# Kernel optimization log

Hardware: AMD Instinct MI355X
Metric: run time of the kernel (lower is better)

## Reference

```python
import jax, jax.numpy as jnp
import numpy as np
import math

B, C, H, W = 32, 64, 128, 128  # x has 2*C channels (real||imag)
EPS = 1e-05


def setup_inputs() -> dict:
    key = jax.random.key(0)
    x = jax.random.normal(key, (B, 2 * C, H, W), dtype=jnp.float32)
    g = 1.0 / math.sqrt(2.0)
    gamma = jnp.tile(jnp.array([[g, 0.0], [0.0, g]], dtype=jnp.float32), (C, 1, 1))
    beta = jnp.zeros((C, 2, 1), dtype=jnp.float32)
    return {"x": x, "gamma": gamma, "beta": beta}


def reference(x, gamma, beta):
    # Training-branch complex batchnorm: whiten with inverse sqrt of 2x2 covariance.
    c = gamma.shape[0]
    xr, xi = x[:, :c], x[:, c:]
    mr = jnp.mean(xr, axis=(0, 2, 3), keepdims=True)
    mi = jnp.mean(xi, axis=(0, 2, 3), keepdims=True)
    xrc = xr - mr
    xic = xi - mi
    d = xr.shape[0] * xr.shape[2] * xr.shape[3] - 1  # unbiased denominator
    covRR = jnp.sum(xrc * xrc, axis=(0, 2, 3)) / d
    covII = jnp.sum(xic * xic, axis=(0, 2, 3)) / d
    covRI = jnp.sum(xrc * xic, axis=(0, 2, 3)) / d
    covIR = covRI  # cov(x_imag, x_real) == cov(x_real, x_imag)
    # cov_matrix per torch stacking: M[c] = [[RR, IR], [RI, II]] + eps*I
    m00 = covRR + EPS
    m01 = covIR
    m10 = covRI
    m11 = covII + EPS
    # sqrtm exactly as in source (including its nonstandard t and full-matrix s add)
    tau = m00 + m11
    delta = m00 * m11 - m01 * m10
    s = jnp.sqrt(delta)
    t = jnp.sqrt(tau + 2.0 * delta)
    q00 = (m00 + s) / t
    q01 = (m01 + s) / t
    q10 = (m10 + s) / t
    q11 = (m11 + s) / t
    # closed-form 2x2 inverse of sqrt matrix
    det = q00 * q11 - q01 * q10
    invV = jnp.stack(
        [jnp.stack([q11, -q01], axis=-1), jnp.stack([-q10, q00], axis=-1)],
        axis=-2,
    ) / det[:, None, None]  # (C, 2, 2)
    # fuse gamma @ invV into a single per-channel 2x2 transform
    A = jnp.einsum('cij,cjk->cik', gamma, invV)  # (C, 2, 2)
    a00 = A[:, 0, 0][None, :, None, None]
    a01 = A[:, 0, 1][None, :, None, None]
    a10 = A[:, 1, 0][None, :, None, None]
    a11 = A[:, 1, 1][None, :, None, None]
    b0 = beta[:, 0, 0][None, :, None, None]
    b1 = beta[:, 1, 0][None, :, None, None]
    yr = a00 * xrc + a01 * xic + b0
    yi = a10 * xrc + a11 * xic + b1
    return jnp.concatenate([yr, yi], axis=1)
```

## Files before the change

### kernel.cpp

```cpp
#include <hip/hip_runtime.h>
#include <math.h>

constexpr int B  = 32;
constexpr int C  = 64;
constexpr int H  = 128;
constexpr int W  = 128;
constexpr int HW = H * W;
constexpr int SB = 2 * C * HW;
constexpr float EPS = 1e-5f;

typedef float v4f __attribute__((ext_vector_type(4)));

__global__ __launch_bounds__(256) void k_partial(const float* __restrict__ x,
                                                 float* __restrict__ part) {
    const int c = blockIdx.x;
    const int b = blockIdx.y;
    const float* __restrict__ xr = x + (size_t)b * SB + (size_t)c * HW;
    const float* __restrict__ xi = xr + (size_t)C * HW;
    const int tid = threadIdx.x;

    float sr = 0.f, si = 0.f, srr = 0.f, sii = 0.f, sri = 0.f;

#pragma unroll
    for (int it = 0; it < HW / (256 * 4); ++it) {
        const int idx = (it * 256 + tid) * 4;
        const v4f r = *reinterpret_cast<const v4f*>(xr + idx);
        const v4f i = *reinterpret_cast<const v4f*>(xi + idx);
        sr  += r.x + r.y + r.z + r.w;
        si  += i.x + i.y + i.z + i.w;
        srr += r.x * r.x + r.y * r.y + r.z * r.z + r.w * r.w;
        sii += i.x * i.x + i.y * i.y + i.z * i.z + i.w * i.w;
        sri += r.x * i.x + r.y * i.y + r.z * i.z + r.w * i.w;
    }

#pragma unroll
    for (int off = 32; off > 0; off >>= 1) {
        sr  += __shfl_down(sr,  off);
        si  += __shfl_down(si,  off);
        srr += __shfl_down(srr, off);
        sii += __shfl_down(sii, off);
        sri += __shfl_down(sri, off);
    }

    __shared__ float smem[4][5];
    const int wave = tid >> 6;
    const int lane = tid & 63;
    if (lane == 0) {
        smem[wave][0] = sr;  smem[wave][1] = si;  smem[wave][2] = srr;
        smem[wave][3] = sii; smem[wave][4] = sri;
    }
    __syncthreads();
    if (tid == 0) {
        float* dst = part + ((size_t)c * B + b) * 5;
#pragma unroll
        for (int k = 0; k < 5; ++k)
            dst[k] = smem[0][k] + smem[1][k] + smem[2][k] + smem[3][k];
    }
}

__device__ __forceinline__ void channel_coefs(const float* __restrict__ part,
                                              const float* __restrict__ gamma,
                                              const float* __restrict__ beta,
                                              int c,
                                              float& mr, float& mi,
                                              float& a00, float& a01,
                                              float& a10, float& a11,
                                              float& b0, float& b1) {
    float sr = 0.f, si = 0.f, srr = 0.f, sii = 0.f, sri = 0.f;
    const float* p = part + (size_t)c * B * 5;
#pragma unroll
    for (int b = 0; b < B; ++b) {
        sr  += p[b * 5 + 0];
        si  += p[b * 5 + 1];
        srr += p[b * 5 + 2];
        sii += p[b * 5 + 3];
        sri += p[b * 5 + 4];
    }
    const float N    = (float)(B * HW);
    const float invN = 1.f / N;
    mr = sr * invN;
    mi = si * invN;
    const float d = N - 1.f;

    const float covRR = (srr - N * mr * mr) / d;
    const float covII = (sii - N * mi * mi) / d;
    const float covRI = (sri - N * mr * mi) / d;

    const float m00 = covRR + EPS;
    const float m01 = covRI;
    const float m10 = covRI;
    const float m11 = covII + EPS;

    const float tau   = m00 + m11;
    const float delta = m00 * m11 - m01 * m10;
    const float s     = sqrtf(delta);
    const float t     = sqrtf(tau + 2.f * delta);

    const float q00 = (m00 + s) / t;
    const float q01 = (m01 + s) / t;
    const float q10 = (m10 + s) / t;
    const float q11 = (m11 + s) / t;

    const float det    = q00 * q11 - q01 * q10;
    const float invdet = 1.f / det;
    const float v00 =  q11 * invdet;
    const float v01 = -q01 * invdet;
    const float v10 = -q10 * invdet;
    const float v11 =  q00 * invdet;

    const float g00 = gamma[c * 4 + 0];
    const float g01 = gamma[c * 4 + 1];
    const float g10 = gamma[c * 4 + 2];
    const float g11 = gamma[c * 4 + 3];

    a00 = g00 * v00 + g01 * v10;
    a01 = g00 * v01 + g01 * v11;
    a10 = g10 * v00 + g11 * v10;
    a11 = g10 * v01 + g11 * v11;
    b0  = beta[c * 2 + 0];
    b1  = beta[c * 2 + 1];
}

__global__ __launch_bounds__(256) void k_norm(const float* __restrict__ x,
                                              const float* __restrict__ part,
                                              const float* __restrict__ gamma,
                                              const float* __restrict__ beta,
                                              float* __restrict__ out) {
    const int bc = blockIdx.y;
    const int b  = bc / C;
    const int c  = bc % C;

    float mr, mi, a00, a01, a10, a11, b0, b1;
    channel_coefs(part, gamma, beta, c, mr, mi, a00, a01, a10, a11, b0, b1);

    const size_t baseR = (size_t)b * SB + (size_t)c * HW;
    const size_t baseI = baseR + (size_t)C * HW;
    const int idx = (blockIdx.x * 256 + threadIdx.x) * 4;

    const v4f r = __builtin_nontemporal_load(
        reinterpret_cast<const v4f*>(x + baseR + idx));
    const v4f i = __builtin_nontemporal_load(
        reinterpret_cast<const v4f*>(x + baseI + idx));

    v4f yr, yi;
    yr.x = a00 * (r.x - mr) + a01 * (i.x - mi) + b0;
    yr.y = a00 * (r.y - mr) + a01 * (i.y - mi) + b0;
    yr.z = a00 * (r.z - mr) + a01 * (i.z - mi) + b0;
    yr.w = a00 * (r.w - mr) + a01 * (i.w - mi) + b0;
    yi.x = a10 * (r.x - mr) + a11 * (i.x - mi) + b1;
    yi.y = a10 * (r.y - mr) + a11 * (i.y - mi) + b1;
    yi.z = a10 * (r.z - mr) + a11 * (i.z - mi) + b1;
    yi.w = a10 * (r.w - mr) + a11 * (i.w - mi) + b1;

    __builtin_nontemporal_store(yr, reinterpret_cast<v4f*>(out + baseR + idx));
    __builtin_nontemporal_store(yi, reinterpret_cast<v4f*>(out + baseI + idx));
}

extern "C" void kernel_launch(void* const* d_in, const int* in_sizes, int n_in,
                              void* d_out, int out_size, void* d_ws, size_t ws_size,
                              hipStream_t stream) {
    const float* x     = (const float*)d_in[0];
    const float* gamma = (const float*)d_in[1];
    const float* beta  = (const float*)d_in[2];
    float* out = (float*)d_out;

    float* part = (float*)d_ws;

    k_partial<<<dim3(C, B), 256, 0, stream>>>(x, part);
    k_norm<<<dim3(HW / 1024, B * C), 256, 0, stream>>>(x, part, gamma, beta, out);
}
```

Measured before the change: 129.5 us.

## Fuse statistics and whitening into one cooperative kernel with cached tiles

Replaces the two-kernel stats-then-normalize pipeline with a single cooperative kernel of 512 blocks, each handling four channel planes of one batch. A grid-wide sync sits between the statistics pass and the whitening pass. Some of each plane is kept in registers and LDS so the second pass does not re-read it from memory. The cost is a grid barrier, heavy register and LDS use (launch bounds of 2 blocks per CU), and reliance on the cooperative launch succeeding; the old two-kernel path is kept as a fallback if it fails.

```diff
diff --git a/kernel.cpp b/kernel.cpp
--- a/kernel.cpp
+++ b/kernel.cpp
@@ -1,5 +1,8 @@
 #include <hip/hip_runtime.h>
+#include <hip/hip_cooperative_groups.h>
 #include <math.h>
+
+namespace cg = cooperative_groups;
 
 constexpr int B  = 32;
 constexpr int C  = 64;
@@ -9,30 +12,91 @@
 constexpr int SB = 2 * C * HW;
 constexpr float EPS = 1e-5f;
 
+constexpr int NTHR  = 256;
+constexpr int NBLK  = 512;
+constexpr int NIT   = HW / (NTHR * 4);
+constexpr int PAIRS = 4;
+
 typedef float v4f __attribute__((ext_vector_type(4)));
 
-__global__ __launch_bounds__(256) void k_partial(const float* __restrict__ x,
-                                                 float* __restrict__ part) {
-    const int c = blockIdx.x;
-    const int b = blockIdx.y;
-    const float* __restrict__ xr = x + (size_t)b * SB + (size_t)c * HW;
-    const float* __restrict__ xi = xr + (size_t)C * HW;
-    const int tid = threadIdx.x;
-
+struct Coefs { float mr, mi, a00, a01, a10, a11, b0, b1; };
+
+__device__ __forceinline__ Coefs channel_coefs(const float* __restrict__ part,
+                                               const float* __restrict__ gamma,
+                                               const float* __restrict__ beta,
+                                               int c) {
     float sr = 0.f, si = 0.f, srr = 0.f, sii = 0.f, sri = 0.f;
-
-#pragma unroll
-    for (int it = 0; it < HW / (256 * 4); ++it) {
-        const int idx = (it * 256 + tid) * 4;
-        const v4f r = *reinterpret_cast<const v4f*>(xr + idx);
-        const v4f i = *reinterpret_cast<const v4f*>(xi + idx);
-        sr  += r.x + r.y + r.z + r.w;
-        si  += i.x + i.y + i.z + i.w;
-        srr += r.x * r.x + r.y * r.y + r.z * r.z + r.w * r.w;
-        sii += i.x * i.x + i.y * i.y + i.z * i.z + i.w * i.w;
-        sri += r.x * i.x + r.y * i.y + r.z * i.z + r.w * i.w;
-    }
-
+    const float* p = part + (size_t)c * B * 5;
+#pragma unroll
+    for (int b = 0; b < B; ++b) {
+        sr  += p[b * 5 + 0];
+        si  += p[b * 5 + 1];
+        srr += p[b * 5 + 2];
+        sii += p[b * 5 + 3];
+        sri += p[b * 5 + 4];
+    }
+    const float N    = (float)(B * HW);
+    const float invN = 1.f / N;
+    Coefs o;
+    o.mr = sr * invN;
+    o.mi = si * invN;
+    const float d = N - 1.f;
+
+    const float covRR = (srr - N * o.mr * o.mr) / d;
+    const float covII = (sii - N * o.mi * o.mi) / d;
+    const float covRI = (sri - N * o.mr * o.mi) / d;
+
+    const float m00 = covRR + EPS;
+    const float m01 = covRI;
+    const float m10 = covRI;
+    const float m11 = covII + EPS;
+
+    const float tau   = m00 + m11;
+    const float delta = m00 * m11 - m01 * m10;
+    const float s     = sqrtf(delta);
+    const float t     = sqrtf(tau + 2.f * delta);
+
+    const float q00 = (m00 + s) / t;
+    const float q01 = (m01 + s) / t;
+    const float q10 = (m10 + s) / t;
+    const float q11 = (m11 + s) / t;
+
+    const float det    = q00 * q11 - q01 * q10;
+    const float invdet = 1.f / det;
+    const float v00 =  q11 * invdet;
+    const float v01 = -q01 * invdet;
+    const float v10 = -q10 * invdet;
+    const float v11 =  q00 * invdet;
+
+    const float g00 = gamma[c * 4 + 0];
+    const float g01 = gamma[c * 4 + 1];
+    const float g10 = gamma[c * 4 + 2];
+    const float g11 = gamma[c * 4 + 3];
+
+    o.a00 = g00 * v00 + g01 * v10;
+    o.a01 = g00 * v01 + g01 * v11;
+    o.a10 = g10 * v00 + g11 * v10;
+    o.a11 = g10 * v01 + g11 * v11;
+    o.b0  = beta[c * 2 + 0];
+    o.b1  = beta[c * 2 + 1];
+    return o;
+}
+
+__device__ __forceinline__ void accum(const v4f r, const v4f i,
+                                      float& sr, float& si,
+                                      float& srr, float& sii, float& sri) {
+    sr  += r.x + r.y + r.z + r.w;
+    si  += i.x + i.y + i.z + i.w;
+    srr += r.x * r.x + r.y * r.y + r.z * r.z + r.w * r.w;
+    sii += i.x * i.x + i.y * i.y + i.z * i.z + i.w * i.w;
+    sri += r.x * i.x + r.y * i.y + r.z * i.z + r.w * i.w;
+}
+
+__device__ __forceinline__ void reduce_and_store(float sr, float si, float srr,
+                                                 float sii, float sri,
+                                                 float (*red)[5],
+                                                 float* __restrict__ part,
+                                                 int c, int b) {
 #pragma unroll
     for (int off = 32; off > 0; off >>= 1) {
         sr  += __shfl_down(sr,  off);
@@ -41,84 +105,188 @@
         sii += __shfl_down(sii, off);
         sri += __shfl_down(sri, off);
     }
-
-    __shared__ float smem[4][5];
+    const int tid  = threadIdx.x;
     const int wave = tid >> 6;
-    const int lane = tid & 63;
-    if (lane == 0) {
-        smem[wave][0] = sr;  smem[wave][1] = si;  smem[wave][2] = srr;
-        smem[wave][3] = sii; smem[wave][4] = sri;
+    if ((tid & 63) == 0) {
+        red[wave][0] = sr;  red[wave][1] = si;  red[wave][2] = srr;
+        red[wave][3] = sii; red[wave][4] = sri;
     }
     __syncthreads();
     if (tid == 0) {
         float* dst = part + ((size_t)c * B + b) * 5;
 #pragma unroll
         for (int k = 0; k < 5; ++k)
-            dst[k] = smem[0][k] + smem[1][k] + smem[2][k] + smem[3][k];
-    }
-}
-
-__device__ __forceinline__ void channel_coefs(const float* __restrict__ part,
-                                              const float* __restrict__ gamma,
-                                              const float* __restrict__ beta,
-                                              int c,
-                                              float& mr, float& mi,
-                                              float& a00, float& a01,
-                                              float& a10, float& a11,
-                                              float& b0, float& b1) {
+            dst[k] = red[0][k] + red[1][k] + red[2][k] + red[3][k];
+    }
+    __syncthreads();
+}
+
+__device__ __forceinline__ v4f whiten4(const v4f r, const v4f i, const Coefs& k) {
+    v4f y;
+    y.x = k.a00 * (r.x - k.mr) + k.a01 * (i.x - k.mi) + k.b0;
+    y.y = k.a00 * (r.y - k.mr) + k.a01 * (i.y - k.mi) + k.b0;
+    y.z = k.a00 * (r.z - k.mr) + k.a01 * (i.z - k.mi) + k.b0;
+    y.w = k.a00 * (r.w - k.mr) + k.a01 * (i.w - k.mi) + k.b0;
+    return y;
+}
+__device__ __forceinline__ v4f whiten4i(const v4f r, const v4f i, const Coefs& k) {
+    v4f y;
+    y.x = k.a10 * (r.x - k.mr) + k.a11 * (i.x - k.mi) + k.b1;
+    y.y = k.a10 * (r.y - k.mr) + k.a11 * (i.y - k.mi) + k.b1;
+    y.z = k.a10 * (r.z - k.mr) + k.a11 * (i.z - k.mi) + k.b1;
+    y.w = k.a10 * (r.w - k.mr) + k.a11 * (i.w - k.mi) + k.b1;
+    return y;
+}
+
+__global__ __launch_bounds__(NTHR, 2) void k_fused(const float* __restrict__ x,
+                                                   const float* __restrict__ gamma,
+                                                   const float* __restrict__ beta,
+                                                   float* __restrict__ part,
+                                                   float* __restrict__ out) {
+    __shared__ v4f ldsR[2][4 * NTHR];
+    __shared__ v4f ldsI[2][4 * NTHR];
+    __shared__ float red[PAIRS][4][5];
+
+    const int tid   = threadIdx.x;
+    const int bid   = blockIdx.x;
+    const int pair0 = PAIRS * bid;
+    const int b     = pair0 >> 6;
+    const int cbase = pair0 & 63;
+
+    const float* xr[PAIRS];
+    const float* xi[PAIRS];
+#pragma unroll
+    for (int p = 0; p < PAIRS; ++p) {
+        xr[p] = x + (size_t)b * SB + (size_t)(cbase + p) * HW;
+        xi[p] = xr[p] + (size_t)C * HW;
+    }
+
+    v4f rr[8], ri[8];
+    {
+        float sr = 0.f, si = 0.f, srr = 0.f, sii = 0.f, sri = 0.f;
+#pragma unroll
+        for (int it = 0; it < 8; ++it) {
+            const int idx = (it * NTHR + tid) * 4;
+            rr[it] = *reinterpret_cast<const v4f*>(xr[0] + idx);
+            ri[it] = *reinterpret_cast<const v4f*>(xi[0] + idx);
+            accum(rr[it], ri[it], sr, si, srr, sii, sri);
+        }
+#pragma unroll
+        for (int it = 8; it < NIT; ++it) {
+            const int idx = (it * NTHR + tid) * 4;
+            const v4f r = *reinterpret_cast<const v4f*>(xr[0] + idx);
+            const v4f i = *reinterpret_cast<const v4f*>(xi[0] + idx);
+            accum(r, i, sr, si, srr, sii, sri);
+        }
+        reduce_and_store(sr, si, srr, sii, sri, red[0], part, cbase + 0, b);
+    }
+
+#pragma unroll
+    for (int p = 1; p <= 2; ++p) {
+        float sr = 0.f, si = 0.f, srr = 0.f, sii = 0.f, sri = 0.f;
+#pragma unroll
+        for (int it = 0; it < 4; ++it) {
+            const int idx = (it * NTHR + tid) * 4;
+            const v4f r = *reinterpret_cast<const v4f*>(xr[p] + idx);
+            const v4f i = *reinterpret_cast<const v4f*>(xi[p] + idx);
+            ldsR[p - 1][it * NTHR + tid] = r;
+            ldsI[p - 1][it * NTHR + tid] = i;
+            accum(r, i, sr, si, srr, sii, sri);
+        }
+#pragma unroll
+        for (int it = 4; it < NIT; ++it) {
+            const int idx = (it * NTHR + tid) * 4;
+            const v4f r = *reinterpret_cast<const v4f*>(xr[p] + idx);
+            const v4f i = *reinterpret_cast<const v4f*>(xi[p] + idx);
+            accum(r, i, sr, si, srr, sii, sri);
+        }
+        reduce_and_store(sr, si, srr, sii, sri, red[p], part, cbase + p, b);
+    }
+
+    {
+        float sr = 0.f, si = 0.f, srr = 0.f, sii = 0.f, sri = 0.f;
+#pragma unroll
+        for (int it = 0; it < NIT; ++it) {
+            const int idx = (it * NTHR + tid) * 4;
+            const v4f r = *reinterpret_cast<const v4f*>(xr[3] + idx);
+            const v4f i = *reinterpret_cast<const v4f*>(xi[3] + idx);
+            accum(r, i, sr, si, srr, sii, sri);
+        }
+        reduce_and_store(sr, si, srr, sii, sri, red[3], part, cbase + 3, b);
+    }
+
+    __threadfence();
+    cg::this_grid().sync();
+
+    const Coefs k0 = channel_coefs(part, gamma, beta, cbase + 0);
+    const Coefs k1 = channel_coefs(part, gamma, beta, cbase + 1);
+    const Coefs k2 = channel_coefs(part, gamma, beta, cbase + 2);
+    const Coefs k3 = channel_coefs(part, gamma, beta, cbase + 3);
+
+    float* orp[PAIRS];
+    float* oip[PAIRS];
+#pragma unroll
+    for (int p = 0; p < PAIRS; ++p) {
+        orp[p] = out + (size_t)b * SB + (size_t)(cbase + p) * HW;
+        oip[p] = orp[p] + (size_t)C * HW;
+    }
+
+#pragma unroll
+    for (int it = 0; it < NIT; ++it) {
+        const int idx = (it * NTHR + tid) * 4;
+        v4f r, i;
+        if (it < 8) { r = rr[it]; i = ri[it]; }
+        else {
+            r = __builtin_nontemporal_load(reinterpret_cast<const v4f*>(xr[0] + idx));
+            i = __builtin_nontemporal_load(reinterpret_cast<const v4f*>(xi[0] + idx));
+        }
+        __builtin_nontemporal_store(whiten4(r, i, k0),  reinterpret_cast<v4f*>(orp[0] + idx));
+        __builtin_nontemporal_store(whiten4i(r, i, k0), reinterpret_cast<v4f*>(oip[0] + idx));
+    }
+#pragma unroll
+    for (int p = 1; p <= 2; ++p) {
+        const Coefs& kk = (p == 1) ? k1 : k2;
+#pragma unroll
+        for (int it = 0; it < NIT; ++it) {
+            const int idx = (it * NTHR + tid) * 4;
+            v4f r, i;
+            if (it < 4) { r = ldsR[p - 1][it * NTHR + tid]; i = ldsI[p - 1][it * NTHR + tid]; }
+            else {
+                r = __builtin_nontemporal_load(reinterpret_cast<const v4f*>(xr[p] + idx));
+                i = __builtin_nontemporal_load(reinterpret_cast<const v4f*>(xi[p] + idx));
+            }
+            __builtin_nontemporal_store(whiten4(r, i, kk),  reinterpret_cast<v4f*>(orp[p] + idx));
+            __builtin_nontemporal_store(whiten4i(r, i, kk), reinterpret_cast<v4f*>(oip[p] + idx));
+        }
+    }
+#pragma unroll
+    for (int it = 0; it < NIT; ++it) {
+        const int idx = (it * NTHR + tid) * 4;
+        const v4f r = __builtin_nontemporal_load(reinterpret_cast<const v4f*>(xr[3] + idx));
+        const v4f i = __builtin_nontemporal_load(reinterpret_cast<const v4f*>(xi[3] + idx));
+        __builtin_nontemporal_store(whiten4(r, i, k3),  reinterpret_cast<v4f*>(orp[3] + idx));
+        __builtin_nontemporal_store(whiten4i(r, i, k3), reinterpret_cast<v4f*>(oip[3] + idx));
+    }
+}
+
+__global__ __launch_bounds__(256) void k_partial(const float* __restrict__ x,
+                                                 float* __restrict__ part) {
+    const int c = blockIdx.x;
+    const int b = blockIdx.y;
+    const float* __restrict__ pxr = x + (size_t)b * SB + (size_t)c * HW;
+    const float* __restrict__ pxi = pxr + (size_t)C * HW;
+    const int tid = threadIdx.x;
+
     float sr = 0.f, si = 0.f, srr = 0.f, sii = 0.f, sri = 0.f;
-    const float* p = part + (size_t)c * B * 5;
-#pragma unroll
-    for (int b = 0; b < B; ++b) {
-        sr  += p[b * 5 + 0];
-        si  += p[b * 5 + 1];
-        srr += p[b * 5 + 2];
-        sii += p[b * 5 + 3];
-        sri += p[b * 5 + 4];
-    }
-    const float N    = (float)(B * HW);
-    const float invN = 1.f / N;
-    mr = sr * invN;
-    mi = si * invN;
-    const float d = N - 1.f;
-
-    const float covRR = (srr - N * mr * mr) / d;
-    const float covII = (sii - N * mi * mi) / d;
-    const float covRI = (sri - N * mr * mi) / d;
-
-    const float m00 = covRR + EPS;
-    const float m01 = covRI;
-    const float m10 = covRI;
-    const float m11 = covII + EPS;
-
-    const float tau   = m00 + m11;
-    const float delta = m00 * m11 - m01 * m10;
-    const float s     = sqrtf(delta);
-    const float t     = sqrtf(tau + 2.f * delta);
-
-    const float q00 = (m00 + s) / t;
-    const float q01 = (m01 + s) / t;
-    const float q10 = (m10 + s) / t;
-    const float q11 = (m11 + s) / t;
-
-    const float det    = q00 * q11 - q01 * q10;
-    const float invdet = 1.f / det;
-    const float v00 =  q11 * invdet;
-    const float v01 = -q01 * invdet;
-    const float v10 = -q10 * invdet;
-    const float v11 =  q00 * invdet;
-
-    const float g00 = gamma[c * 4 + 0];
-    const float g01 = gamma[c * 4 + 1];
-    const float g10 = gamma[c * 4 + 2];
-    const float g11 = gamma[c * 4 + 3];
-
-    a00 = g00 * v00 + g01 * v10;
-    a01 = g00 * v01 + g01 * v11;
-    a10 = g10 * v00 + g11 * v10;
-    a11 = g10 * v01 + g11 * v11;
-    b0  = beta[c * 2 + 0];
-    b1  = beta[c * 2 + 1];
+#pragma unroll
+    for (int it = 0; it < NIT; ++it) {
+        const int idx = (it * 256 + tid) * 4;
+        const v4f r = *reinterpret_cast<const v4f*>(pxr + idx);
+        const v4f i = *reinterpret_cast<const v4f*>(pxi + idx);
+        accum(r, i, sr, si, srr, sii, sri);
+    }
+    __shared__ float red[4][5];
+    reduce_and_store(sr, si, srr, sii, sri, red, part, c, b);
 }
 
 __global__ __launch_bounds__(256) void k_norm(const float* __restrict__ x,
@@ -129,31 +297,16 @@
     const int bc = blockIdx.y;
     const int b  = bc / C;
     const int c  = bc % C;
-
-    float mr, mi, a00, a01, a10, a11, b0, b1;
-    channel_coefs(part, gamma, beta, c, mr, mi, a00, a01, a10, a11, b0, b1);
+    const Coefs k = channel_coefs(part, gamma, beta, c);
 
     const size_t baseR = (size_t)b * SB + (size_t)c * HW;
     const size_t baseI = baseR + (size_t)C * HW;
     const int idx = (blockIdx.x * 256 + threadIdx.x) * 4;
 
-    const v4f r = __builtin_nontemporal_load(
-        reinterpret_cast<const v4f*>(x + baseR + idx));
-    const v4f i = __builtin_nontemporal_load(
-        reinterpret_cast<const v4f*>(x + baseI + idx));
-
-    v4f yr, yi;
-    yr.x = a00 * (r.x - mr) + a01 * (i.x - mi) + b0;
-    yr.y = a00 * (r.y - mr) + a01 * (i.y - mi) + b0;
-    yr.z = a00 * (r.z - mr) + a01 * (i.z - mi) + b0;
-    yr.w = a00 * (r.w - mr) + a01 * (i.w - mi) + b0;
-    yi.x = a10 * (r.x - mr) + a11 * (i.x - mi) + b1;
-    yi.y = a10 * (r.y - mr) + a11 * (i.y - mi) + b1;
-    yi.z = a10 * (r.z - mr) + a11 * (i.z - mi) + b1;
-    yi.w = a10 * (r.w - mr) + a11 * (i.w - mi) + b1;
-
-    __builtin_nontemporal_store(yr, reinterpret_cast<v4f*>(out + baseR + idx));
-    __builtin_nontemporal_store(yi, reinterpret_cast<v4f*>(out + baseI + idx));
+    const v4f r = __builtin_nontemporal_load(reinterpret_cast<const v4f*>(x + baseR + idx));
+    const v4f i = __builtin_nontemporal_load(reinterpret_cast<const v4f*>(x + baseI + idx));
+    __builtin_nontemporal_store(whiten4(r, i, k),  reinterpret_cast<v4f*>(out + baseR + idx));
+    __builtin_nontemporal_store(whiten4i(r, i, k), reinterpret_cast<v4f*>(out + baseI + idx));
 }
 
 extern "C" void kernel_launch(void* const* d_in, const int* in_sizes, int n_in,
@@ -162,10 +315,16 @@
     const float* x     = (const float*)d_in[0];
     const float* gamma = (const float*)d_in[1];
     const float* beta  = (const float*)d_in[2];
-    float* out = (float*)d_out;
-
+    float* out  = (float*)d_out;
     float* part = (float*)d_ws;
 
-    k_partial<<<dim3(C, B), 256, 0, stream>>>(x, part);
-    k_norm<<<dim3(HW / 1024, B * C), 256, 0, stream>>>(x, part, gamma, beta, out);
-}
+    void* args[] = {(void*)&x, (void*)&gamma, (void*)&beta,
+                    (void*)&part, (void*)&out};
+    hipError_t err = hipLaunchCooperativeKernel((const void*)k_fused,
+                                                dim3(NBLK), dim3(NTHR),
+                                                args, 0, stream);
+    if (err != hipSuccess) {
+        k_partial<<<dim3(C, B), 256, 0, stream>>>(x, part);
+        k_norm<<<dim3(HW / 1024, B * C), 256, 0, stream>>>(x, part, gamma, beta, out);
+    }
+}
```

Result: slower. 273.1 us (+110.9%).
